# Optimization experiments

Hardware: AMD Instinct MI355X
Metric: run time of the kernel (lower is better)

Reference implementation:

```python
import jax, jax.numpy as jnp
import numpy as np

IN_DIM = 128
OUT_DIM = 128
DEGREE = 3
BATCH = 8192


def setup_inputs() -> dict:
    key = jax.random.key(0)
    k1, k2 = jax.random.split(key)
    x = jax.random.normal(k1, (BATCH, IN_DIM), dtype=jnp.float32)
    # coeff ~ 0.1*randn, shape [out_dim*in_dim, degree+1]
    coeff = 0.1 * jax.random.normal(k2, (OUT_DIM * IN_DIM, DEGREE + 1), dtype=jnp.float32)
    return {"x": x, "coeff": coeff}


def reference(x, coeff):
    # x: [B, in_dim], coeff: [out_dim*in_dim, D+1]
    # Original tiles x to [out_dim*in_dim, B]; edge i = (o*in_dim + j) uses x[:, j].
    # out[i,b] = sum_d coeff[i,d] * x[b, i % in_dim]**d, then sum over in_dim.
    B, in_dim = x.shape
    D1 = coeff.shape[-1]
    out_dim = coeff.shape[0] // in_dim
    exps = jnp.arange(D1, dtype=x.dtype)
    powed = x[:, :, None] ** exps            # [B, in_dim, D+1]
    c = coeff.reshape(out_dim, in_dim, D1)    # [out_dim, in_dim, D+1]
    # per-edge polynomial eval fused with sum over in_dim
    y = jnp.einsum('bid,oid->bo', powed, c)   # [B, out_dim]
    return y
```

## Files before the change

kernel.cpp:

```cpp
#include <hip/hip_runtime.h>


#define BATCH   8192
#define IN_DIM  128
#define OUT_DIM 128
#define KDIM    512
#define KP      384
#define M_BLK   64
#define N_BLK   32
#define WPAD    392
#define APAD    392

typedef __attribute__((ext_vector_type(8))) short bf16x8;
typedef __attribute__((ext_vector_type(4))) float f32x4;

__device__ inline unsigned short f2bf(float f) {
    union { float f; unsigned int u; } v; v.f = f;
    unsigned int u = v.u;
    u += 0x7FFFu + ((u >> 16) & 1u);
    return (unsigned short)(u >> 16);
}

#if defined(__has_builtin)
#if __has_builtin(__builtin_amdgcn_cvt_pk_bf16_f32)
#define HAVE_HW_PKBF16 1
#endif
#endif

#ifdef HAVE_HW_PKBF16
typedef __attribute__((ext_vector_type(2))) __bf16 bf16x2_t;
__device__ inline unsigned int pk2(float a, float b) {
    bf16x2_t r = __builtin_amdgcn_cvt_pk_bf16_f32(a, b);
    union { bf16x2_t v; unsigned int u; } c; c.v = r; return c.u;
}
#else
__device__ inline unsigned int pk2(float a, float b) {
    return (unsigned int)f2bf(a) | ((unsigned int)f2bf(b) << 16);
}
#endif

__global__ __launch_bounds__(256, 2) void kan_mfma(const float* __restrict__ x,
                                                   const float* __restrict__ coeff,
                                                   float* __restrict__ out) {
    __shared__ __align__(16) unsigned short W_lds[N_BLK * WPAD];
    __shared__ __align__(16) unsigned short A_lds[M_BLK * APAD];
    __shared__ float bias_lds[N_BLK];

    const int t    = threadIdx.x;
    const int w    = t >> 6;
    const int lane = t & 63;
    const int q    = lane >> 4;
    const int r    = lane & 15;
    const int m0   = blockIdx.x * M_BLK;
    const int n0   = blockIdx.y * N_BLK;

    {
        const int jl = lane * 2;
        #pragma unroll
        for (int i = 0; i < 8; ++i) {
            const int row = i * 4 + w;
            const float* cp = &coeff[(size_t)(n0 + row) * KDIM + (size_t)jl * 4];
            const float4 cA = *(const float4*)cp;
            const float4 cB = *(const float4*)(cp + 4);
            unsigned short* Wr = &W_lds[row * WPAD + jl];
            *(unsigned int*)(Wr)       = pk2(cA.y, cB.y);
            *(unsigned int*)(Wr + 128) = pk2(cA.z, cB.z);
            *(unsigned int*)(Wr + 256) = pk2(cA.w, cB.w);
        }
    }

    {
        const int o = w * 8 + (lane >> 3);
        const float* cp = &coeff[(size_t)(n0 + o) * KDIM + (size_t)(lane & 7) * 64];
        float bsum = 0.f;
        #pragma unroll
        for (int jj = 0; jj < 16; ++jj) bsum += cp[jj * 4];
        bsum += __shfl_xor(bsum, 1);
        bsum += __shfl_xor(bsum, 2);
        bsum += __shfl_xor(bsum, 4);
        if ((lane & 7) == 0) bias_lds[o] = bsum;
    }

    #pragma unroll
    for (int i = 0; i < 8; ++i) {
        const int f   = i * 256 + t;
        const int row = f >> 5;
        const int c4  = f & 31;
        const float4 v = *(const float4*)&x[(size_t)(m0 + row) * IN_DIM + c4 * 4];
        const float x2a = v.x * v.x, x2b = v.y * v.y;
        const float x2c = v.z * v.z, x2d = v.w * v.w;
        uint2 s1, s2, s3;
        s1.x = pk2(v.x, v.y);         s1.y = pk2(v.z, v.w);
        s2.x = pk2(x2a, x2b);         s2.y = pk2(x2c, x2d);
        s3.x = pk2(x2a * v.x, x2b * v.y); s3.y = pk2(x2c * v.z, x2d * v.w);
        unsigned short* Ar = &A_lds[row * APAD + c4 * 4];
        *(uint2*)(Ar)       = s1;
        *(uint2*)(Ar + 128) = s2;
        *(uint2*)(Ar + 256) = s3;
    }

    __syncthreads();

    f32x4 acc0 = {0.f, 0.f, 0.f, 0.f};
    f32x4 acc1 = {0.f, 0.f, 0.f, 0.f};
    const unsigned short* Ap = &A_lds[(w * 16 + r) * APAD + q * 8];
    const unsigned short* B0 = &W_lds[r        * WPAD + q * 8];
    const unsigned short* B1 = &W_lds[(16 + r) * WPAD + q * 8];
    #pragma unroll
    for (int u = 0; u < 12; ++u) {
        const bf16x8 av = *(const bf16x8*)(Ap + u * 32);
        const bf16x8 b0 = *(const bf16x8*)(B0 + u * 32);
        const bf16x8 b1 = *(const bf16x8*)(B1 + u * 32);
        acc0 = __builtin_amdgcn_mfma_f32_16x16x32_bf16(av, b0, acc0, 0, 0, 0);
        acc1 = __builtin_amdgcn_mfma_f32_16x16x32_bf16(av, b1, acc1, 0, 0, 0);
    }

    const float bb0 = bias_lds[r];
    const float bb1 = bias_lds[16 + r];
    float* obase = out + (size_t)(m0 + w * 16 + q * 4) * OUT_DIM + n0 + r;
    #pragma unroll
    for (int rr = 0; rr < 4; ++rr) {
        obase[rr * OUT_DIM]      = acc0[rr] + bb0;
        obase[rr * OUT_DIM + 16] = acc1[rr] + bb1;
    }
}

extern "C" void kernel_launch(void* const* d_in, const int* in_sizes, int n_in,
                              void* d_out, int out_size, void* d_ws, size_t ws_size,
                              hipStream_t stream) {
    const float* x     = (const float*)d_in[0];
    const float* coeff = (const float*)d_in[1];
    float* out = (float*)d_out;

    dim3 grid(BATCH / M_BLK, OUT_DIM / N_BLK);
    kan_mfma<<<grid, 256, 0, stream>>>(x, coeff, out);
}
```

Measured before the change: 63.50 us.

## Split A staging into power planes and overlap x^2/x^3 compute with first MFMAs

Loads all x rows into registers up front, writes only the x plane to LDS, runs the first four MFMA steps, then computes and stores the x^2 and x^3 planes before a second barrier and the remaining steps. The bias sum is folded into the coefficient load loop using wave-wide shuffles, which removes a separate strided read pass over coeff. A is laid out as three planes with a smaller row pad. The aim is to hide the power computation behind matrix work, at the cost of an extra barrier and more live registers for the eight float4 x values.

```diff
diff --git a/kernel.cpp b/kernel.cpp
--- a/kernel.cpp
+++ b/kernel.cpp
@@ -5,11 +5,11 @@
 #define IN_DIM  128
 #define OUT_DIM 128
 #define KDIM    512
-#define KP      384
 #define M_BLK   64
 #define N_BLK   32
 #define WPAD    392
-#define APAD    392
+#define APAD2   136
+#define PLANE   (M_BLK * APAD2)
 
 typedef __attribute__((ext_vector_type(8))) short bf16x8;
 typedef __attribute__((ext_vector_type(4))) float f32x4;
@@ -43,7 +43,7 @@
                                                    const float* __restrict__ coeff,
                                                    float* __restrict__ out) {
     __shared__ __align__(16) unsigned short W_lds[N_BLK * WPAD];
-    __shared__ __align__(16) unsigned short A_lds[M_BLK * APAD];
+    __shared__ __align__(16) unsigned short A_lds[3 * PLANE];
     __shared__ float bias_lds[N_BLK];
 
     const int t    = threadIdx.x;
@@ -54,61 +54,75 @@
     const int m0   = blockIdx.x * M_BLK;
     const int n0   = blockIdx.y * N_BLK;
 
+    const int arow = t >> 5;
+    const int ac4  = t & 31;
+    float4 xv[8];
+    #pragma unroll
+    for (int i = 0; i < 8; ++i)
+        xv[i] = *(const float4*)&x[(size_t)(m0 + i * 8 + arow) * IN_DIM + ac4 * 4];
+
     {
         const int jl = lane * 2;
         #pragma unroll
         for (int i = 0; i < 8; ++i) {
-            const int row = i * 4 + w;
-            const float* cp = &coeff[(size_t)(n0 + row) * KDIM + (size_t)jl * 4];
+            const int wrow = i * 4 + w;
+            const float* cp = &coeff[(size_t)(n0 + wrow) * KDIM + (size_t)jl * 4];
             const float4 cA = *(const float4*)cp;
             const float4 cB = *(const float4*)(cp + 4);
-            unsigned short* Wr = &W_lds[row * WPAD + jl];
+            unsigned short* Wr = &W_lds[wrow * WPAD + jl];
             *(unsigned int*)(Wr)       = pk2(cA.y, cB.y);
             *(unsigned int*)(Wr + 128) = pk2(cA.z, cB.z);
             *(unsigned int*)(Wr + 256) = pk2(cA.w, cB.w);
+            float b = cA.x + cB.x;
+            b += __shfl_xor(b, 1);  b += __shfl_xor(b, 2);
+            b += __shfl_xor(b, 4);  b += __shfl_xor(b, 8);
+            b += __shfl_xor(b, 16); b += __shfl_xor(b, 32);
+            if (lane == 0) bias_lds[wrow] = b;
         }
-    }
-
-    {
-        const int o = w * 8 + (lane >> 3);
-        const float* cp = &coeff[(size_t)(n0 + o) * KDIM + (size_t)(lane & 7) * 64];
-        float bsum = 0.f;
-        #pragma unroll
-        for (int jj = 0; jj < 16; ++jj) bsum += cp[jj * 4];
-        bsum += __shfl_xor(bsum, 1);
-        bsum += __shfl_xor(bsum, 2);
-        bsum += __shfl_xor(bsum, 4);
-        if ((lane & 7) == 0) bias_lds[o] = bsum;
     }
 
     #pragma unroll
     for (int i = 0; i < 8; ++i) {
-        const int f   = i * 256 + t;
-        const int row = f >> 5;
-        const int c4  = f & 31;
-        const float4 v = *(const float4*)&x[(size_t)(m0 + row) * IN_DIM + c4 * 4];
-        const float x2a = v.x * v.x, x2b = v.y * v.y;
-        const float x2c = v.z * v.z, x2d = v.w * v.w;
-        uint2 s1, s2, s3;
-        s1.x = pk2(v.x, v.y);         s1.y = pk2(v.z, v.w);
-        s2.x = pk2(x2a, x2b);         s2.y = pk2(x2c, x2d);
-        s3.x = pk2(x2a * v.x, x2b * v.y); s3.y = pk2(x2c * v.z, x2d * v.w);
-        unsigned short* Ar = &A_lds[row * APAD + c4 * 4];
-        *(uint2*)(Ar)       = s1;
-        *(uint2*)(Ar + 128) = s2;
-        *(uint2*)(Ar + 256) = s3;
+        uint2 s1;
+        s1.x = pk2(xv[i].x, xv[i].y);
+        s1.y = pk2(xv[i].z, xv[i].w);
+        *(uint2*)&A_lds[(i * 8 + arow) * APAD2 + ac4 * 4] = s1;
     }
-
     __syncthreads();
 
     f32x4 acc0 = {0.f, 0.f, 0.f, 0.f};
     f32x4 acc1 = {0.f, 0.f, 0.f, 0.f};
-    const unsigned short* Ap = &A_lds[(w * 16 + r) * APAD + q * 8];
+    const unsigned short* Ap = &A_lds[(w * 16 + r) * APAD2 + q * 8];
     const unsigned short* B0 = &W_lds[r        * WPAD + q * 8];
     const unsigned short* B1 = &W_lds[(16 + r) * WPAD + q * 8];
+
     #pragma unroll
-    for (int u = 0; u < 12; ++u) {
+    for (int u = 0; u < 4; ++u) {
         const bf16x8 av = *(const bf16x8*)(Ap + u * 32);
+        const bf16x8 b0 = *(const bf16x8*)(B0 + u * 32);
+        const bf16x8 b1 = *(const bf16x8*)(B1 + u * 32);
+        acc0 = __builtin_amdgcn_mfma_f32_16x16x32_bf16(av, b0, acc0, 0, 0, 0);
+        acc1 = __builtin_amdgcn_mfma_f32_16x16x32_bf16(av, b1, acc1, 0, 0, 0);
+    }
+
+    #pragma unroll
+    for (int i = 0; i < 8; ++i) {
+        const float x2a = xv[i].x * xv[i].x, x2b = xv[i].y * xv[i].y;
+        const float x2c = xv[i].z * xv[i].z, x2d = xv[i].w * xv[i].w;
+        uint2 s2, s3;
+        s2.x = pk2(x2a, x2b);              s2.y = pk2(x2c, x2d);
+        s3.x = pk2(x2a * xv[i].x, x2b * xv[i].y);
+        s3.y = pk2(x2c * xv[i].z, x2d * xv[i].w);
+        unsigned short* Ar = &A_lds[(i * 8 + arow) * APAD2 + ac4 * 4];
+        *(uint2*)(Ar + PLANE)     = s2;
+        *(uint2*)(Ar + 2 * PLANE) = s3;
+    }
+    __syncthreads();
+
+    #pragma unroll
+    for (int u = 4; u < 12; ++u) {
+        const unsigned short* Apl = Ap + (u >> 2) * PLANE + (u & 3) * 32;
+        const bf16x8 av = *(const bf16x8*)(Apl);
         const bf16x8 b0 = *(const bf16x8*)(B0 + u * 32);
         const bf16x8 b1 = *(const bf16x8*)(B1 + u * 32);
         acc0 = __builtin_amdgcn_mfma_f32_16x16x32_bf16(av, b0, acc0, 0, 0, 0);
```

New measurement: 62.85 us. No clear change (-1.0%).
